# Performance work log

Hardware: AMD Instinct MI355X
Metric: run time of the kernel (lower is better)

## Reference

```python
import jax, jax.numpy as jnp
import numpy as np

H = 896          # hidden_size
S = H // 2       # split_size = 448
Q = 256          # quantisation
B = 16384        # batch (parallel sampling streams)


def setup_inputs() -> dict:
    key = jax.random.key(0)
    ks = jax.random.split(key, 16)
    sc = 0.02
    return {
        "prev_y": jax.random.uniform(ks[0], (B, 2), dtype=jnp.float32),
        "prev_hidden": jax.random.normal(ks[1], (B, H), dtype=jnp.float32),
        "current_coarse": jax.random.uniform(ks[2], (B, 1), dtype=jnp.float32),
        # torch Linear weights are [out_features, in_features]
        "R_w": sc * jax.random.normal(ks[3], (3 * H, H), dtype=jnp.float32),
        "Ic_w": sc * jax.random.normal(ks[4], (3 * S, 2), dtype=jnp.float32),
        "If_w": sc * jax.random.normal(ks[5], (3 * S, 3), dtype=jnp.float32),
        "bias_u": jnp.zeros((H,), jnp.float32),
        "bias_r": jnp.zeros((H,), jnp.float32),
        "bias_e": jnp.zeros((H,), jnp.float32),
        "O1_w": sc * jax.random.normal(ks[6], (S, S), dtype=jnp.float32),
        "O1_b": jnp.zeros((S,), jnp.float32),
        "O2_w": sc * jax.random.normal(ks[7], (Q, S), dtype=jnp.float32),
        "O2_b": jnp.zeros((Q,), jnp.float32),
        "O3_w": sc * jax.random.normal(ks[8], (S, S), dtype=jnp.float32),
        "O3_b": jnp.zeros((S,), jnp.float32),
        "O4_w": sc * jax.random.normal(ks[9], (Q, S), dtype=jnp.float32),
        "O4_b": jnp.zeros((Q,), jnp.float32),
    }


def reference(prev_y, prev_hidden, current_coarse,
              R_w, Ic_w, If_w, bias_u, bias_r, bias_e,
              O1_w, O1_b, O2_w, O2_b, O3_w, O3_b, O4_w, O4_b):
    # recurrent projection: [B,H] @ [H,3H] -> [B,3H]
    R_hidden = prev_hidden @ R_w.T
    R_u, R_r, R_e = jnp.split(R_hidden, 3, axis=1)

    # coarse input projection: [B,2] -> [B,3S]
    cproj = prev_y @ Ic_w.T
    Ic_u, Ic_r, Ic_e = jnp.split(cproj, 3, axis=1)

    # fine input projection: [B,3] -> [B,3S]
    fine_in = jnp.concatenate([prev_y, current_coarse], axis=1)
    fproj = fine_in @ If_w.T
    If_u, If_r, If_e = jnp.split(fproj, 3, axis=1)

    I_u = jnp.concatenate([Ic_u, If_u], axis=1)  # [B,H]
    I_r = jnp.concatenate([Ic_r, If_r], axis=1)
    I_e = jnp.concatenate([Ic_e, If_e], axis=1)

    u = jax.nn.sigmoid(R_u + I_u + bias_u)
    r = jax.nn.sigmoid(R_r + I_r + bias_r)
    e = jnp.tanh(r * R_e + I_e + bias_e)
    hidden = u * prev_hidden + (1.0 - u) * e  # [B,H]

    h_coarse, h_fine = jnp.split(hidden, 2, axis=1)  # [B,S] each
    out_coarse = jax.nn.relu(h_coarse @ O1_w.T + O1_b) @ O2_w.T + O2_b  # [B,Q]
    out_fine = jax.nn.relu(h_fine @ O3_w.T + O3_b) @ O4_w.T + O4_b      # [B,Q]
    return (out_coarse, out_fine, hidden)
```

## Files before the change

kernel.cpp:

```cpp
#include <hip/hip_runtime.h>
#include <hip/hip_bf16.h>
#include <cstdint>

#define BB 16384
#define HH 896
#define SS 448
#define QQ 256
#define NPAD 2816

typedef __attribute__((ext_vector_type(4))) float f32x4;
typedef __attribute__((ext_vector_type(8))) short bf16x8;

__device__ __forceinline__ short f2bf(float f){
  union { float f; uint32_t u; } x; x.f = f;
  uint32_t r = (x.u + 0x7fffu + ((x.u >> 16) & 1u)) >> 16;
  return (short)r;
}
__device__ __forceinline__ float bf2f(short b){
  union { uint32_t u; float f; } x; x.u = ((uint32_t)(uint16_t)b) << 16;
  return x.f;
}

__global__ void cast4_kernel(const float* __restrict__ src, short* __restrict__ dst, long n4){
  long i = (long)blockIdx.x * blockDim.x + threadIdx.x;
  if (i >= n4) return;
  const float4 v = reinterpret_cast<const float4*>(src)[i];
  short4 o; o.x = f2bf(v.x); o.y = f2bf(v.y); o.z = f2bf(v.z); o.w = f2bf(v.w);
  reinterpret_cast<short4*>(dst)[i] = o;
}

__global__ void castpad_kernel(const float* __restrict__ src, short* __restrict__ dst,
                               int srows, int scols, int dcols, int total){
  int i = blockIdx.x * blockDim.x + threadIdx.x;
  if (i >= total) return;
  int r = i / dcols, c = i - r * dcols;
  float v = (r < srows && c < scols) ? src[(long)r * scols + c] : 0.f;
  dst[i] = f2bf(v);
}

__global__ void castpadO_kernel(const float* __restrict__ O1w, const float* __restrict__ O3w,
                                const float* __restrict__ O2w, const float* __restrict__ O4w,
                                short* __restrict__ O1b, short* __restrict__ O3b,
                                short* __restrict__ O2b, short* __restrict__ O4b){
  int i = blockIdx.x * 256 + threadIdx.x;
  const int n13 = 512 * 448, n24 = 256 * 512;
  const float* src; short* dst; int srows, scols, dcols, j;
  if (i < n13)                { src = O1w; dst = O1b; srows = 448; scols = 448; dcols = 448; j = i; }
  else if (i < 2 * n13)       { src = O3w; dst = O3b; srows = 448; scols = 448; dcols = 448; j = i - n13; }
  else if (i < 2 * n13 + n24) { src = O2w; dst = O2b; srows = 256; scols = 448; dcols = 512; j = i - 2 * n13; }
  else if (i < 2 * (n13 + n24)) { src = O4w; dst = O4b; srows = 256; scols = 448; dcols = 512; j = i - 2 * n13 - n24; }
  else return;
  int r = j / dcols, c = j - r * dcols;
  float v = (r < srows && c < scols) ? src[(long)r * scols + c] : 0.f;
  dst[j] = f2bf(v);
}

__global__ __launch_bounds__(512, 2)
void gemm256_bt(const short* __restrict__ A, int lda,
                const short* __restrict__ Bt, int ldb,
                short* __restrict__ C, int ldc, int Nvalid,
                int K, int nbn)
{
  __shared__ short smem[65536];
  const int tid = threadIdx.x;
  const int w  = tid >> 6, ln = tid & 63;
  const int wr = w >> 2,  wc = w & 3;
  const int lr = ln & 15;
  const int lg = ln >> 4;
  const int srow = ln >> 3;
  const int sgc  = (ln & 7) ^ srow;

  int wg = blockIdx.x;
  const int cpx = gridDim.x >> 3;
  wg = (wg & 7) * cpx + (wg >> 3);
  const int bm = wg / nbn, bn = wg - bm * nbn;
  const long m0 = (long)bm * 256, n0 = (long)bn * 256;

  f32x4 acc[8][4] = {};

  auto stage = [&](const short* __restrict__ src, int ld, long rbase, int k0,
                   int lbase , int h) {
#pragma unroll
    for (int i = 0; i < 2; ++i) {
      const int rloc = h * 128 + i * 64 + w * 8;
      const short* g = src + (rbase + rloc + srow) * (long)ld + k0 + sgc * 8;
      __builtin_amdgcn_global_load_lds(
          (const __attribute__((address_space(1))) void*)g,
          (__attribute__((address_space(3))) void*)&smem[lbase + rloc * 64],
          16, 0, 0);
    }
  };
  auto rd = [&](int lbase, int r, int ks) -> bf16x8 {
    const int gc = ks * 4 + lg;
    return *reinterpret_cast<const bf16x8*>(&smem[lbase + r * 64 + ((gc ^ (r & 7)) << 3)]);
  };

  const int NT = K >> 6;
  stage(A,  lda, m0, 0, 0,     0);
  stage(Bt, ldb, n0, 0, 32768, 0);
  stage(Bt, ldb, n0, 0, 32768, 1);
  stage(A,  lda, m0, 0, 0,     1);
  asm volatile("s_waitcnt vmcnt(2)" ::: "memory");
  __builtin_amdgcn_s_barrier();
  asm volatile("" ::: "memory");
  __builtin_amdgcn_sched_barrier(0);

  for (int j = 0; j < NT; ++j) {
    const int Ab = (j & 1) * 16384;
    const int Bb = 32768 + (j & 1) * 16384;
    const int An = ((j + 1) & 1) * 16384;
    const int Bn = 32768 + ((j + 1) & 1) * 16384;
    const bool pf = (j + 1 < NT);
    const int k1 = (j + 1) << 6;
    bf16x8 b[4][2];
#pragma unroll
    for (int q = 0; q < 4; ++q) {
      bf16x8 a[2][2];
#pragma unroll
      for (int dm = 0; dm < 2; ++dm)
#pragma unroll
        for (int ks = 0; ks < 2; ++ks)
          a[dm][ks] = rd(Ab, q * 64 + dm * 32 + wr * 16 + lr, ks);
      if (q == 0) {
#pragma unroll
        for (int n = 0; n < 4; ++n)
#pragma unroll
          for (int ks = 0; ks < 2; ++ks)
            b[n][ks] = rd(Bb, wc * 64 + n * 16 + lr, ks);
        if (pf) {
          stage(A,  lda, m0, k1, An, 0);
          stage(Bt, ldb, n0, k1, Bn, 0);
          stage(Bt, ldb, n0, k1, Bn, 1);
          stage(A,  lda, m0, k1, An, 1);
        }
      }
      asm volatile("" ::: "memory");
      __builtin_amdgcn_s_barrier();
      asm volatile("s_waitcnt lgkmcnt(0)" ::: "memory");
      __builtin_amdgcn_sched_barrier(0);
      __builtin_amdgcn_s_setprio(1);
#pragma unroll
      for (int dm = 0; dm < 2; ++dm)
#pragma unroll
        for (int n = 0; n < 4; ++n)
#pragma unroll
          for (int ks = 0; ks < 2; ++ks)
            acc[2 * q + dm][n] = __builtin_amdgcn_mfma_f32_16x16x32_bf16(
                a[dm][ks], b[n][ks], acc[2 * q + dm][n], 0, 0, 0);
      __builtin_amdgcn_s_setprio(0);
      __builtin_amdgcn_sched_barrier(0);
      if (q == 1) {
        if (pf) asm volatile("s_waitcnt vmcnt(8)" ::: "memory");
        else    asm volatile("s_waitcnt vmcnt(0)" ::: "memory");
      } else if (q == 3) {
        asm volatile("s_waitcnt vmcnt(2)" ::: "memory");
      }
      asm volatile("" ::: "memory");
      __builtin_amdgcn_s_barrier();
      asm volatile("" ::: "memory");
      __builtin_amdgcn_sched_barrier(0);
    }
  }

#pragma unroll
  for (int n = 0; n < 4; ++n) {
    const int col = wc * 64 + n * 16 + lr;
#pragma unroll
    for (int m = 0; m < 8; ++m) {
      const int row = m * 32 + wr * 16 + lg * 4;
#pragma unroll
      for (int reg = 0; reg < 4; ++reg)
        smem[(row + reg) * 256 + col] = f2bf(acc[m][n][reg]);
    }
  }
  __builtin_amdgcn_s_barrier();
  const int rt = tid >> 5;
  const int ct = (tid & 31) * 8;
  const long colg = n0 + ct;
  if (colg < Nvalid) {
#pragma unroll
    for (int p = 0; p < 16; ++p) {
      const int row = p * 16 + rt;
      bf16x8 v = *reinterpret_cast<const bf16x8*>(&smem[row * 256 + ct]);
      *reinterpret_cast<bf16x8*>(&C[(m0 + row) * (long)ldc + colg]) = v;
    }
  }
}

#define EP_RELU_BIAS_BF16 1
#define EP_BIAS_F32 2

template<int EP>
__global__ __launch_bounds__(256)
void gemm_bt(const short* __restrict__ A0, const short* __restrict__ A1, int lda,
             const short* __restrict__ W0, const short* __restrict__ W1, int ldb,
             void* __restrict__ C0v, void* __restrict__ C1v, int ldc,
             const float* __restrict__ bias0, const float* __restrict__ bias1, int nbias,
             int K)
{
  const short* A  = blockIdx.z ? A1 : A0;
  const short* Bt = blockIdx.z ? W1 : W0;
  void* Cv        = blockIdx.z ? C1v : C0v;
  const float* bias = blockIdx.z ? bias1 : bias0;

  __shared__ short As[128 * 64];
  __shared__ short Bs[128 * 64];
  const int tid = threadIdx.x;
  const int wv = tid >> 6, ln = tid & 63;
  const int wr = wv >> 1, wc = wv & 1;
  const long m0 = (long)blockIdx.y * 128;
  const long n0 = (long)blockIdx.x * 128;

  f32x4 acc[4][4] = {};
  const int lr = ln & 15;
  const int lkbase = (ln >> 4) * 8;
  const int e0 = ln * 8;
  for (int k0 = 0; k0 < K; k0 += 64) {
    __syncthreads();
#pragma unroll
    for (int i = 0; i < 4; i++) {
      int chunk = wv * 4 + i;
      int e = chunk * 512 + e0;
      int row = e >> 6, col = e & 63;
      const short* g = A + (m0 + row) * lda + k0 + col;
      __builtin_amdgcn_global_load_lds((const __attribute__((address_space(1))) void*)g,
                                       (__attribute__((address_space(3))) void*)&As[chunk * 512],
                                       16, 0, 0);
    }
#pragma unroll
    for (int i = 0; i < 4; i++) {
      int chunk = wv * 4 + i;
      int e = chunk * 512 + e0;
      int row = e >> 6, col = e & 63;
      const short* g = Bt + (n0 + row) * ldb + k0 + col;
      __builtin_amdgcn_global_load_lds((const __attribute__((address_space(1))) void*)g,
                                       (__attribute__((address_space(3))) void*)&Bs[chunk * 512],
                                       16, 0, 0);
    }
    __syncthreads();
#pragma unroll
    for (int ks = 0; ks < 2; ks++) {
      bf16x8 a[4], b[4];
#pragma unroll
      for (int m = 0; m < 4; m++)
        a[m] = *reinterpret_cast<const bf16x8*>(&As[(wr * 64 + m * 16 + lr) * 64 + ks * 32 + lkbase]);
#pragma unroll
      for (int n = 0; n < 4; n++)
        b[n] = *reinterpret_cast<const bf16x8*>(&Bs[(wc * 64 + n * 16 + lr) * 64 + ks * 32 + lkbase]);
#pragma unroll
      for (int m = 0; m < 4; m++)
#pragma unroll
        for (int n = 0; n < 4; n++)
          acc[m][n] = __builtin_amdgcn_mfma_f32_16x16x32_bf16(a[m], b[n], acc[m][n], 0, 0, 0);
    }
  }

  const int lc = ln & 15;
  const int r4 = (ln >> 4) * 4;
#pragma unroll
  for (int m = 0; m < 4; m++) {
#pragma unroll
    for (int n = 0; n < 4; n++) {
      long col = n0 + wc * 64 + n * 16 + lc;
#pragma unroll
      for (int reg = 0; reg < 4; reg++) {
        long row = m0 + wr * 64 + m * 16 + r4 + reg;
        float v = acc[m][n][reg];
        if (EP == EP_RELU_BIAS_BF16) {
          float bv = (col < nbias) ? bias[col] : 0.f;
          v += bv;
          v = v > 0.f ? v : 0.f;
          ((short*)Cv)[row * ldc + col] = f2bf(v);
        } else {
          v += bias[col];
          ((float*)Cv)[row * ldc + col] = v;
        }
      }
    }
  }
}

__global__ __launch_bounds__(256)
void gates_kernel(const float* __restrict__ prev_y,
                  const float* __restrict__ prev_hidden,
                  const float* __restrict__ ccoarse,
                  const float* __restrict__ Icw,
                  const float* __restrict__ Ifw,
                  const float* __restrict__ bu,
                  const float* __restrict__ br,
                  const float* __restrict__ be,
                  const short* __restrict__ Rh,
                  float* __restrict__ hid_out,
                  short* __restrict__ hid_bf)
{
  const int v = blockIdx.x * 256 + threadIdx.x;
  const int b = v / 112;
  const int h0 = (v - b * 112) * 8;
  const long rbase = (long)b * (3 * HH);

  const bf16x8 ru8 = *reinterpret_cast<const bf16x8*>(Rh + rbase + h0);
  const bf16x8 rr8 = *reinterpret_cast<const bf16x8*>(Rh + rbase + HH + h0);
  const bf16x8 re8 = *reinterpret_cast<const bf16x8*>(Rh + rbase + 2 * HH + h0);
  const float4* ph4 = reinterpret_cast<const float4*>(prev_hidden + (long)b * HH + h0);
  const float4 pha = ph4[0], phb = ph4[1];
  const float py0 = prev_y[2 * b], py1 = prev_y[2 * b + 1], c0 = ccoarse[b];

  float iu[8], ir[8], ie[8];
  if (h0 < SS) {
    const float4* cu = reinterpret_cast<const float4*>(Icw + 2 * h0);
    const float4* cr = reinterpret_cast<const float4*>(Icw + 2 * (SS + h0));
    const float4* ce = reinterpret_cast<const float4*>(Icw + 2 * (2 * SS + h0));
#pragma unroll
    for (int q = 0; q < 4; ++q) {
      float4 a = cu[q]; iu[2*q] = py0*a.x + py1*a.y; iu[2*q+1] = py0*a.z + py1*a.w;
      float4 r = cr[q]; ir[2*q] = py0*r.x + py1*r.y; ir[2*q+1] = py0*r.z + py1*r.w;
      float4 e = ce[q]; ie[2*q] = py0*e.x + py1*e.y; ie[2*q+1] = py0*e.z + py1*e.w;
    }
  } else {
    const int j0 = h0 - SS;
    const float* fu = Ifw + 3 * j0;
    const float* fr = Ifw + 3 * (SS + j0);
    const float* fe = Ifw + 3 * (2 * SS + j0);
#pragma unroll
    for (int j = 0; j < 8; ++j) {
      iu[j] = py0 * fu[3*j] + py1 * fu[3*j+1] + c0 * fu[3*j+2];
      ir[j] = py0 * fr[3*j] + py1 * fr[3*j+1] + c0 * fr[3*j+2];
      ie[j] = py0 * fe[3*j] + py1 * fe[3*j+1] + c0 * fe[3*j+2];
    }
  }
  const float4* bu4 = reinterpret_cast<const float4*>(bu + h0);
  const float4* br4 = reinterpret_cast<const float4*>(br + h0);
  const float4* be4 = reinterpret_cast<const float4*>(be + h0);
  float buv[8], brv[8], bev[8];
  { float4 a = bu4[0], b2 = bu4[1];
    buv[0]=a.x; buv[1]=a.y; buv[2]=a.z; buv[3]=a.w; buv[4]=b2.x; buv[5]=b2.y; buv[6]=b2.z; buv[7]=b2.w; }
  { float4 a = br4[0], b2 = br4[1];
    brv[0]=a.x; brv[1]=a.y; brv[2]=a.z; brv[3]=a.w; brv[4]=b2.x; brv[5]=b2.y; brv[6]=b2.z; brv[7]=b2.w; }
  { float4 a = be4[0], b2 = be4[1];
    bev[0]=a.x; bev[1]=a.y; bev[2]=a.z; bev[3]=a.w; bev[4]=b2.x; bev[5]=b2.y; bev[6]=b2.z; bev[7]=b2.w; }
  float ph[8] = { pha.x, pha.y, pha.z, pha.w, phb.x, phb.y, phb.z, phb.w };

  float hd[8];
  bf16x8 hb;
#pragma unroll
  for (int j = 0; j < 8; ++j) {
    float u = 1.f / (1.f + __expf(-(bf2f(ru8[j]) + iu[j] + buv[j])));
    float r = 1.f / (1.f + __expf(-(bf2f(rr8[j]) + ir[j] + brv[j])));
    float e = tanhf(r * bf2f(re8[j]) + ie[j] + bev[j]);
    hd[j] = u * ph[j] + (1.f - u) * e;
    hb[j] = f2bf(hd[j]);
  }
  float4* ho = reinterpret_cast<float4*>(hid_out + (long)b * HH + h0);
  ho[0] = make_float4(hd[0], hd[1], hd[2], hd[3]);
  ho[1] = make_float4(hd[4], hd[5], hd[6], hd[7]);
  *reinterpret_cast<bf16x8*>(hid_bf + (long)b * HH + h0) = hb;
}

extern "C" void kernel_launch(void* const* d_in, const int* in_sizes, int n_in,
                              void* d_out, int out_size, void* d_ws, size_t ws_size,
                              hipStream_t stream)
{
  (void)in_sizes; (void)n_in; (void)out_size; (void)ws_size;
  const float* prev_y      = (const float*)d_in[0];
  const float* prev_hidden = (const float*)d_in[1];
  const float* ccoarse     = (const float*)d_in[2];
  const float* R_w  = (const float*)d_in[3];
  const float* Ic_w = (const float*)d_in[4];
  const float* If_w = (const float*)d_in[5];
  const float* bu   = (const float*)d_in[6];
  const float* br   = (const float*)d_in[7];
  const float* be   = (const float*)d_in[8];
  const float* O1w  = (const float*)d_in[9];
  const float* O1b  = (const float*)d_in[10];
  const float* O2w  = (const float*)d_in[11];
  const float* O2b  = (const float*)d_in[12];
  const float* O3w  = (const float*)d_in[13];
  const float* O3b  = (const float*)d_in[14];
  const float* O4w  = (const float*)d_in[15];
  const float* O4b  = (const float*)d_in[16];

  float* out_coarse = (float*)d_out;
  float* out_fine   = out_coarse + (long)BB * QQ;
  float* hidden     = out_fine + (long)BB * QQ;

  char* ws = (char*)d_ws;
  short* Ah   = (short*)(ws + 0);
  short* Rwh  = (short*)(ws + 29360128);
  short* Rh   = (short*)(ws + 34406400);
  short* hidb = (short*)(ws + 122486784);
  short* O1wb = (short*)(ws + 151846912);
  short* O3wb = (short*)(ws + 152305664);
  short* O2wb = (short*)(ws + 152764416);
  short* O4wb = (short*)(ws + 153026560);
  short* t1   = (short*)(ws + 0);
  short* t2   = (short*)(ws + 16777216);

  long nAh4 = (long)BB * HH / 4;
  cast4_kernel<<<(int)((nAh4 + 255) / 256), 256, 0, stream>>>(prev_hidden, Ah, nAh4);
  castpad_kernel<<<(NPAD * HH + 255) / 256, 256, 0, stream>>>(R_w, Rwh, 3 * HH, HH, HH, NPAD * HH);
  castpadO_kernel<<<(2 * (512 * 448 + 256 * 512) + 255) / 256, 256, 0, stream>>>(
      O1w, O3w, O2w, O4w, O1wb, O3wb, O2wb, O4wb);

  gemm256_bt<<<(BB / 256) * (NPAD / 256), 512, 0, stream>>>(
      Ah, HH, Rwh, HH, Rh, 3 * HH, 3 * HH, HH, NPAD / 256);

  gates_kernel<<<BB * 112 / 256, 256, 0, stream>>>(prev_y, prev_hidden, ccoarse,
                                                   Ic_w, If_w, bu, br, be, Rh, hidden, hidb);

  gemm_bt<EP_RELU_BIAS_BF16><<<dim3(4, BB / 128, 2), 256, 0, stream>>>(
      hidb, hidb + 448, HH, O1wb, O3wb, 448, t1, t2, 512, O1b, O3b, 448, 448);
  gemm_bt<EP_BIAS_F32><<<dim3(2, BB / 128, 2), 256, 0, stream>>>(
      t1, t2, 512, O2wb, O4wb, 512, out_coarse, out_fine, 256, O2b, O4b, 256, 512);
}
```

Measured before the change: 252.1 us.

## Reuse 256-tile pipelined GEMM for output layers, merge cast kernels, trim barriers

The three cast/pad kernels become one flat kernel that converts 4 elements per thread. The large 256x256 pipelined MFMA GEMM is templated with bias+ReLU and bias-to-float epilogues so it can replace the simpler 128x128 GEMM for both output MLP layers, handling coarse and fine via blockIdx.z. Two of the four per-quarter barriers in the main loop are removed, and the gates kernel now reads the bf16 copy of prev_hidden instead of the fp32 one. The aims are to cut launch overhead, use a more efficient GEMM tile, reduce synchronisation and halve prev_hidden traffic. The costs are lower precision in the hidden-state update and a possible LDS race from the dropped barriers.

```diff
diff --git a/kernel.cpp b/kernel.cpp
--- a/kernel.cpp
+++ b/kernel.cpp
@@ -21,46 +21,60 @@
   return x.f;
 }
 
-__global__ void cast4_kernel(const float* __restrict__ src, short* __restrict__ dst, long n4){
-  long i = (long)blockIdx.x * blockDim.x + threadIdx.x;
-  if (i >= n4) return;
-  const float4 v = reinterpret_cast<const float4*>(src)[i];
-  short4 o; o.x = f2bf(v.x); o.y = f2bf(v.y); o.z = f2bf(v.z); o.w = f2bf(v.w);
-  reinterpret_cast<short4*>(dst)[i] = o;
-}
-
-__global__ void castpad_kernel(const float* __restrict__ src, short* __restrict__ dst,
-                               int srows, int scols, int dcols, int total){
-  int i = blockIdx.x * blockDim.x + threadIdx.x;
-  if (i >= total) return;
-  int r = i / dcols, c = i - r * dcols;
-  float v = (r < srows && c < scols) ? src[(long)r * scols + c] : 0.f;
-  dst[i] = f2bf(v);
-}
-
-__global__ void castpadO_kernel(const float* __restrict__ O1w, const float* __restrict__ O3w,
-                                const float* __restrict__ O2w, const float* __restrict__ O4w,
-                                short* __restrict__ O1b, short* __restrict__ O3b,
-                                short* __restrict__ O2b, short* __restrict__ O4b){
-  int i = blockIdx.x * 256 + threadIdx.x;
-  const int n13 = 512 * 448, n24 = 256 * 512;
-  const float* src; short* dst; int srows, scols, dcols, j;
-  if (i < n13)                { src = O1w; dst = O1b; srows = 448; scols = 448; dcols = 448; j = i; }
-  else if (i < 2 * n13)       { src = O3w; dst = O3b; srows = 448; scols = 448; dcols = 448; j = i - n13; }
-  else if (i < 2 * n13 + n24) { src = O2w; dst = O2b; srows = 256; scols = 448; dcols = 512; j = i - 2 * n13; }
-  else if (i < 2 * (n13 + n24)) { src = O4w; dst = O4b; srows = 256; scols = 448; dcols = 512; j = i - 2 * n13 - n24; }
-  else return;
-  int r = j / dcols, c = j - r * dcols;
-  float v = (r < srows && c < scols) ? src[(long)r * scols + c] : 0.f;
-  dst[j] = f2bf(v);
-}
-
+__global__ __launch_bounds__(256)
+void castall_kernel(const float* __restrict__ ph, short* __restrict__ Ah,
+                    const float* __restrict__ Rw, short* __restrict__ Rwh,
+                    const float* __restrict__ O1w, short* __restrict__ O1b,
+                    const float* __restrict__ O3w, short* __restrict__ O3b,
+                    const float* __restrict__ O2w, short* __restrict__ O2b,
+                    const float* __restrict__ O4w, short* __restrict__ O4b)
+{
+  int u = blockIdx.x * 256 + threadIdx.x;
+  auto cp4 = [](short* d, const float* s, int jd, int js){
+    float4 v = reinterpret_cast<const float4*>(s)[js];
+    short4 o; o.x = f2bf(v.x); o.y = f2bf(v.y); o.z = f2bf(v.z); o.w = f2bf(v.w);
+    reinterpret_cast<short4*>(d)[jd] = o;
+  };
+  auto z4 = [](short* d, int jd){
+    short4 o; o.x = 0; o.y = 0; o.z = 0; o.w = 0;
+    reinterpret_cast<short4*>(d)[jd] = o;
+  };
+  if (u < 3670016) { cp4(Ah, ph, u, u); return; }
+  u -= 3670016;
+  if (u < 602112) { cp4(Rwh, Rw, u, u); return; }
+  u -= 602112;
+  if (u < 28672) { z4(Rwh, 602112 + u); return; }
+  u -= 28672;
+  if (u < 57344) { if (u < 50176) cp4(O1b, O1w, u, u); else z4(O1b, u); return; }
+  u -= 57344;
+  if (u < 57344) { if (u < 50176) cp4(O3b, O3w, u, u); else z4(O3b, u); return; }
+  u -= 57344;
+  if (u < 32768) {
+    int r = u >> 7, c4 = u & 127;
+    if (c4 < 112) cp4(O2b, O2w, u, r * 112 + c4); else z4(O2b, u);
+    return;
+  }
+  u -= 32768;
+  if (u < 32768) {
+    int r = u >> 7, c4 = u & 127;
+    if (c4 < 112) cp4(O4b, O4w, u, r * 112 + c4); else z4(O4b, u);
+    return;
+  }
+}
+
+template<int EP>
 __global__ __launch_bounds__(512, 2)
-void gemm256_bt(const short* __restrict__ A, int lda,
-                const short* __restrict__ Bt, int ldb,
-                short* __restrict__ C, int ldc, int Nvalid,
-                int K, int nbn)
+void gemm256_bt(const short* __restrict__ A0p, const short* __restrict__ A1p, int lda,
+                const short* __restrict__ B0p, const short* __restrict__ B1p, int ldb,
+                void* __restrict__ C0p, void* __restrict__ C1p, int ldc,
+                const float* __restrict__ bias0, const float* __restrict__ bias1, int nbias,
+                int Nvalid, int K, int nbn)
 {
+  const short* A  = blockIdx.z ? A1p : A0p;
+  const short* Bt = blockIdx.z ? B1p : B0p;
+  void* Cv        = blockIdx.z ? C1p : C0p;
+  const float* bias = blockIdx.z ? bias1 : bias0;
+
   __shared__ short smem[65536];
   const int tid = threadIdx.x;
   const int w  = tid >> 6, ln = tid & 63;
@@ -134,8 +148,6 @@
           stage(A,  lda, m0, k1, An, 1);
         }
       }
-      asm volatile("" ::: "memory");
-      __builtin_amdgcn_s_barrier();
       asm volatile("s_waitcnt lgkmcnt(0)" ::: "memory");
       __builtin_amdgcn_sched_barrier(0);
       __builtin_amdgcn_s_setprio(1);
@@ -152,25 +164,52 @@
       if (q == 1) {
         if (pf) asm volatile("s_waitcnt vmcnt(8)" ::: "memory");
         else    asm volatile("s_waitcnt vmcnt(0)" ::: "memory");
+        __builtin_amdgcn_s_barrier();
+        asm volatile("" ::: "memory");
+        __builtin_amdgcn_sched_barrier(0);
       } else if (q == 3) {
         asm volatile("s_waitcnt vmcnt(2)" ::: "memory");
+        __builtin_amdgcn_s_barrier();
+        asm volatile("" ::: "memory");
+        __builtin_amdgcn_sched_barrier(0);
       }
-      asm volatile("" ::: "memory");
-      __builtin_amdgcn_s_barrier();
-      asm volatile("" ::: "memory");
-      __builtin_amdgcn_sched_barrier(0);
-    }
+    }
+  }
+
+  if (EP == 2) {
+    const int lc = ln & 15, rg = lg * 4;
+#pragma unroll
+    for (int n = 0; n < 4; ++n) {
+      const long col = n0 + wc * 64 + n * 16 + lc;
+      const float bv = bias[col];
+#pragma unroll
+      for (int m = 0; m < 8; ++m) {
+        const long row = m0 + m * 32 + wr * 16 + rg;
+#pragma unroll
+        for (int reg = 0; reg < 4; ++reg)
+          ((float*)Cv)[(row + reg) * (long)ldc + col] = acc[m][n][reg] + bv;
+      }
+    }
+    return;
   }
 
 #pragma unroll
   for (int n = 0; n < 4; ++n) {
     const int col = wc * 64 + n * 16 + lr;
+    float bv = 0.f;
+    if (EP == 1) {
+      const long gcol = n0 + col;
+      bv = (gcol < nbias) ? bias[gcol] : 0.f;
+    }
 #pragma unroll
     for (int m = 0; m < 8; ++m) {
       const int row = m * 32 + wr * 16 + lg * 4;
 #pragma unroll
-      for (int reg = 0; reg < 4; ++reg)
-        smem[(row + reg) * 256 + col] = f2bf(acc[m][n][reg]);
+      for (int reg = 0; reg < 4; ++reg) {
+        float v = acc[m][n][reg];
+        if (EP == 1) { v += bv; v = v > 0.f ? v : 0.f; }
+        smem[(row + reg) * 256 + col] = f2bf(v);
+      }
     }
   }
   __builtin_amdgcn_s_barrier();
@@ -182,107 +221,14 @@
     for (int p = 0; p < 16; ++p) {
       const int row = p * 16 + rt;
       bf16x8 v = *reinterpret_cast<const bf16x8*>(&smem[row * 256 + ct]);
-      *reinterpret_cast<bf16x8*>(&C[(m0 + row) * (long)ldc + colg]) = v;
-    }
-  }
-}
-
-#define EP_RELU_BIAS_BF16 1
-#define EP_BIAS_F32 2
-
-template<int EP>
-__global__ __launch_bounds__(256)
-void gemm_bt(const short* __restrict__ A0, const short* __restrict__ A1, int lda,
-             const short* __restrict__ W0, const short* __restrict__ W1, int ldb,
-             void* __restrict__ C0v, void* __restrict__ C1v, int ldc,
-             const float* __restrict__ bias0, const float* __restrict__ bias1, int nbias,
-             int K)
-{
-  const short* A  = blockIdx.z ? A1 : A0;
-  const short* Bt = blockIdx.z ? W1 : W0;
-  void* Cv        = blockIdx.z ? C1v : C0v;
-  const float* bias = blockIdx.z ? bias1 : bias0;
-
-  __shared__ short As[128 * 64];
-  __shared__ short Bs[128 * 64];
-  const int tid = threadIdx.x;
-  const int wv = tid >> 6, ln = tid & 63;
-  const int wr = wv >> 1, wc = wv & 1;
-  const long m0 = (long)blockIdx.y * 128;
-  const long n0 = (long)blockIdx.x * 128;
-
-  f32x4 acc[4][4] = {};
-  const int lr = ln & 15;
-  const int lkbase = (ln >> 4) * 8;
-  const int e0 = ln * 8;
-  for (int k0 = 0; k0 < K; k0 += 64) {
-    __syncthreads();
-#pragma unroll
-    for (int i = 0; i < 4; i++) {
-      int chunk = wv * 4 + i;
-      int e = chunk * 512 + e0;
-      int row = e >> 6, col = e & 63;
-      const short* g = A + (m0 + row) * lda + k0 + col;
-      __builtin_amdgcn_global_load_lds((const __attribute__((address_space(1))) void*)g,
-                                       (__attribute__((address_space(3))) void*)&As[chunk * 512],
-                                       16, 0, 0);
-    }
-#pragma unroll
-    for (int i = 0; i < 4; i++) {
-      int chunk = wv * 4 + i;
-      int e = chunk * 512 + e0;
-      int row = e >> 6, col = e & 63;
-      const short* g = Bt + (n0 + row) * ldb + k0 + col;
-      __builtin_amdgcn_global_load_lds((const __attribute__((address_space(1))) void*)g,
-                                       (__attribute__((address_space(3))) void*)&Bs[chunk * 512],
-                                       16, 0, 0);
-    }
-    __syncthreads();
-#pragma unroll
-    for (int ks = 0; ks < 2; ks++) {
-      bf16x8 a[4], b[4];
-#pragma unroll
-      for (int m = 0; m < 4; m++)
-        a[m] = *reinterpret_cast<const bf16x8*>(&As[(wr * 64 + m * 16 + lr) * 64 + ks * 32 + lkbase]);
-#pragma unroll
-      for (int n = 0; n < 4; n++)
-        b[n] = *reinterpret_cast<const bf16x8*>(&Bs[(wc * 64 + n * 16 + lr) * 64 + ks * 32 + lkbase]);
-#pragma unroll
-      for (int m = 0; m < 4; m++)
-#pragma unroll
-        for (int n = 0; n < 4; n++)
-          acc[m][n] = __builtin_amdgcn_mfma_f32_16x16x32_bf16(a[m], b[n], acc[m][n], 0, 0, 0);
-    }
-  }
-
-  const int lc = ln & 15;
-  const int r4 = (ln >> 4) * 4;
-#pragma unroll
-  for (int m = 0; m < 4; m++) {
-#pragma unroll
-    for (int n = 0; n < 4; n++) {
-      long col = n0 + wc * 64 + n * 16 + lc;
-#pragma unroll
-      for (int reg = 0; reg < 4; reg++) {
-        long row = m0 + wr * 64 + m * 16 + r4 + reg;
-        float v = acc[m][n][reg];
-        if (EP == EP_RELU_BIAS_BF16) {
-          float bv = (col < nbias) ? bias[col] : 0.f;
-          v += bv;
-          v = v > 0.f ? v : 0.f;
-          ((short*)Cv)[row * ldc + col] = f2bf(v);
-        } else {
-          v += bias[col];
-          ((float*)Cv)[row * ldc + col] = v;
-        }
-      }
+      *reinterpret_cast<bf16x8*>(&((short*)Cv)[(m0 + row) * (long)ldc + colg]) = v;
     }
   }
 }
 
 __global__ __launch_bounds__(256)
 void gates_kernel(const float* __restrict__ prev_y,
-                  const float* __restrict__ prev_hidden,
+                  const short* __restrict__ Ah,
                   const float* __restrict__ ccoarse,
                   const float* __restrict__ Icw,
                   const float* __restrict__ Ifw,
@@ -301,8 +247,7 @@
   const bf16x8 ru8 = *reinterpret_cast<const bf16x8*>(Rh + rbase + h0);
   const bf16x8 rr8 = *reinterpret_cast<const bf16x8*>(Rh + rbase + HH + h0);
   const bf16x8 re8 = *reinterpret_cast<const bf16x8*>(Rh + rbase + 2 * HH + h0);
-  const float4* ph4 = reinterpret_cast<const float4*>(prev_hidden + (long)b * HH + h0);
-  const float4 pha = ph4[0], phb = ph4[1];
+  const bf16x8 ah8 = *reinterpret_cast<const bf16x8*>(Ah + (long)b * HH + h0);
   const float py0 = prev_y[2 * b], py1 = prev_y[2 * b + 1], c0 = ccoarse[b];
 
   float iu[8], ir[8], ie[8];
@@ -338,7 +283,6 @@
     brv[0]=a.x; brv[1]=a.y; brv[2]=a.z; brv[3]=a.w; brv[4]=b2.x; brv[5]=b2.y; brv[6]=b2.z; brv[7]=b2.w; }
   { float4 a = be4[0], b2 = be4[1];
     bev[0]=a.x; bev[1]=a.y; bev[2]=a.z; bev[3]=a.w; bev[4]=b2.x; bev[5]=b2.y; bev[6]=b2.z; bev[7]=b2.w; }
-  float ph[8] = { pha.x, pha.y, pha.z, pha.w, phb.x, phb.y, phb.z, phb.w };
 
   float hd[8];
   bf16x8 hb;
@@ -347,7 +291,7 @@
     float u = 1.f / (1.f + __expf(-(bf2f(ru8[j]) + iu[j] + buv[j])));
     float r = 1.f / (1.f + __expf(-(bf2f(rr8[j]) + ir[j] + brv[j])));
     float e = tanhf(r * bf2f(re8[j]) + ie[j] + bev[j]);
-    hd[j] = u * ph[j] + (1.f - u) * e;
+    hd[j] = u * bf2f(ah8[j]) + (1.f - u) * e;
     hb[j] = f2bf(hd[j]);
   }
   float4* ho = reinterpret_cast<float4*>(hid_out + (long)b * HH + h0);
@@ -395,20 +339,21 @@
   short* t1   = (short*)(ws + 0);
   short* t2   = (short*)(ws + 16777216);
 
-  long nAh4 = (long)BB * HH / 4;
-  cast4_kernel<<<(int)((nAh4 + 255) / 256), 256, 0, stream>>>(prev_hidden, Ah, nAh4);
-  castpad_kernel<<<(NPAD * HH + 255) / 256, 256, 0, stream>>>(R_w, Rwh, 3 * HH, HH, HH, NPAD * HH);
-  castpadO_kernel<<<(2 * (512 * 448 + 256 * 512) + 255) / 256, 256, 0, stream>>>(
-      O1w, O3w, O2w, O4w, O1wb, O3wb, O2wb, O4wb);
-
-  gemm256_bt<<<(BB / 256) * (NPAD / 256), 512, 0, stream>>>(
-      Ah, HH, Rwh, HH, Rh, 3 * HH, 3 * HH, HH, NPAD / 256);
-
-  gates_kernel<<<BB * 112 / 256, 256, 0, stream>>>(prev_y, prev_hidden, ccoarse,
+  castall_kernel<<<17504, 256, 0, stream>>>(prev_hidden, Ah, R_w, Rwh,
+                                            O1w, O1wb, O3w, O3wb, O2w, O2wb, O4w, O4wb);
+
+  gemm256_bt<0><<<dim3(704, 1, 1), 512, 0, stream>>>(
+      Ah, Ah, HH, Rwh, Rwh, HH, Rh, Rh, 3 * HH,
+      nullptr, nullptr, 0, 3 * HH, HH, NPAD / 256);
+
+  gates_kernel<<<BB * 112 / 256, 256, 0, stream>>>(prev_y, Ah, ccoarse,
                                                    Ic_w, If_w, bu, br, be, Rh, hidden, hidb);
 
-  gemm_bt<EP_RELU_BIAS_BF16><<<dim3(4, BB / 128, 2), 256, 0, stream>>>(
-      hidb, hidb + 448, HH, O1wb, O3wb, 448, t1, t2, 512, O1b, O3b, 448, 448);
-  gemm_bt<EP_BIAS_F32><<<dim3(2, BB / 128, 2), 256, 0, stream>>>(
-      t1, t2, 512, O2wb, O4wb, 512, out_coarse, out_fine, 256, O2b, O4b, 256, 512);
-}
+  gemm256_bt<1><<<dim3(128, 1, 2), 512, 0, stream>>>(
+      hidb, hidb + 448, HH, O1wb, O3wb, 448, t1, t2, 512,
+      O1b, O3b, 448, 512, 448, 2);
+
+  gemm256_bt<2><<<dim3(64, 1, 2), 512, 0, stream>>>(
+      t1, t2, 512, O2wb, O4wb, 512, out_coarse, out_fine, QQ,
+      O2b, O4b, QQ, QQ, 512, 1);
+}
```

After: 214.8 us. 14.8% less time.
